# Kernel tuning notes

Measured on AMD Instinct MI355X. Metric: run time of the kernel, lower is better.

Reference implementation:

```python
import jax, jax.numpy as jnp
import numpy as np

N = 100000   # nodes
E = 1600000  # edges
D = 64       # hidden_channels
H = 2 * D    # MLP expansion
L = 4        # num_layers
G = 64       # graphs in batch
OUT = 1      # out_channels
LN_EPS = 1e-5


def layer_norm(h, gamma, beta):
    mu = jnp.mean(h, axis=-1, keepdims=True)
    var = jnp.var(h, axis=-1, keepdims=True)
    return (h - mu) * jax.lax.rsqrt(var + LN_EPS) * gamma + beta


def setup_inputs() -> dict:
    key = jax.random.key(0)
    ks = jax.random.split(key, 16)
    s = 0.05
    x = jax.random.normal(ks[0], (N, D), jnp.float32)
    edge_index = jax.random.randint(ks[1], (2, E), 0, N)
    batch = jnp.sort(jax.random.randint(ks[2], (N,), 0, G))
    # lin_in
    W_in = jax.random.normal(ks[3], (D, D), jnp.float32) * s
    b_in = jnp.zeros((D,), jnp.float32)
    # per-layer GINConv params (stacked over L layers)
    eps = jnp.zeros((L,), jnp.float32)
    W1 = jax.random.normal(ks[4], (L, D, H), jnp.float32) * s
    b1 = jnp.zeros((L, H), jnp.float32)
    gamma = jnp.ones((L, H), jnp.float32)
    beta = jnp.zeros((L, H), jnp.float32)
    W2 = jax.random.normal(ks[5], (L, H, D), jnp.float32) * s
    b2 = jnp.zeros((L, D), jnp.float32)
    # lin_out MLP
    Wo1 = jax.random.normal(ks[6], (D, H), jnp.float32) * s
    bo1 = jnp.zeros((H,), jnp.float32)
    Wo2 = jax.random.normal(ks[7], (H, OUT), jnp.float32) * s
    bo2 = jnp.zeros((OUT,), jnp.float32)
    return {
        "x": x, "W_in": W_in, "b_in": b_in, "eps": eps,
        "W1": W1, "b1": b1, "gamma": gamma, "beta": beta,
        "W2": W2, "b2": b2, "Wo1": Wo1, "bo1": bo1,
        "Wo2": Wo2, "bo2": bo2,
        "edge_index": edge_index, "batch": batch,
    }


def gin_conv(h, edge_index, eps_l, W1_l, b1_l, gamma_l, beta_l, W2_l, b2_l):
    src = edge_index[0]  # x_j
    dst = edge_index[1]  # aggregation target i
    # message = relu(x_j); aggr = scatter-add into dst
    agg = jax.ops.segment_sum(jax.nn.relu(h[src]), dst, num_segments=N)
    z = (1.0 + eps_l) * h + agg
    z = z @ W1_l + b1_l
    z = jax.nn.relu(layer_norm(z, gamma_l, beta_l))
    return z @ W2_l + b2_l


def reference(x, W_in, b_in, eps, W1, b1, gamma, beta, W2, b2,
              Wo1, bo1, Wo2, bo2, edge_index, batch):
    h = x @ W_in + b_in  # [N, D]
    for i in range(L):
        h = h + gin_conv(h, edge_index, eps[i], W1[i], b1[i],
                         gamma[i], beta[i], W2[i], b2[i])
        # dropout p=0.0 -> identity
    pooled = jax.ops.segment_sum(h, batch, num_segments=G)  # [G, D]
    out = jax.nn.relu(pooled @ Wo1 + bo1) @ Wo2 + bo2        # [G, OUT]
    return out.reshape(-1)
```

## Files before the change

### kernel.cpp

```cpp
#include <hip/hip_runtime.h>
#include <hip/hip_bf16.h>

#define NN 100000
#define NE 1600000
#define DD 64
#define HH 128
#define NLAYERS 4
#define NGRAPH 64
#define NBUCKET 782
#define NCHUNK 391
#define NTOT (NBUCKET * NCHUNK)

typedef __attribute__((ext_vector_type(8))) short bf16x8;
typedef __attribute__((ext_vector_type(4))) float f32x4;
typedef __attribute__((ext_vector_type(2))) float f32x2;

__device__ inline unsigned short bf16bits(float v) {
  return __bfloat16_as_ushort(__float2bfloat16(v));
}
__device__ inline float lo16(unsigned int u) { return __uint_as_float(u << 16); }
__device__ inline float hi16(unsigned int u) { return __uint_as_float(u & 0xFFFF0000u); }
__device__ inline float b2f(unsigned short u) { return __uint_as_float(((unsigned int)u) << 16); }


__global__ void k_hist(const int* __restrict__ dst, int* __restrict__ hist) {
  __shared__ int lh[NBUCKET];
  int t = threadIdx.x;
  int blk = blockIdx.x;
  for (int i = t; i < NBUCKET; i += 256) lh[i] = 0;
  __syncthreads();
  int cb = blk * 4096;
  int end = min(cb + 4096, NE);
  for (int i = cb + t; i < end; i += 256)
    atomicAdd(&lh[dst[i] >> 7], 1);
  __syncthreads();
  for (int i = t; i < NBUCKET; i += 256)
    hist[i * NCHUNK + blk] = lh[i];
}

__global__ void k_scan1(const int* __restrict__ in, int* __restrict__ out,
                        int* __restrict__ bsum, int n) {
  __shared__ int s[256];
  int t = threadIdx.x;
  int i = blockIdx.x * 256 + t;
  int v = (i < n) ? in[i] : 0;
  s[t] = v;
  __syncthreads();
  for (int off = 1; off < 256; off <<= 1) {
    int x = (t >= off) ? s[t - off] : 0;
    __syncthreads();
    s[t] += x;
    __syncthreads();
  }
  if (i < n) out[i] = s[t] - v;
  if (t == 255) bsum[blockIdx.x] = s[255];
}

__global__ void k_scan2b(int* bsum, int nb) {
  __shared__ int s[256];
  int t = threadIdx.x;
  int base = t * 5;
  int v[5];
  int sum = 0;
#pragma unroll
  for (int j = 0; j < 5; j++) {
    int i = base + j;
    v[j] = (i < nb) ? bsum[i] : 0;
    sum += v[j];
  }
  s[t] = sum;
  __syncthreads();
  for (int off = 1; off < 256; off <<= 1) {
    int x = (t >= off) ? s[t - off] : 0;
    __syncthreads();
    s[t] += x;
    __syncthreads();
  }
  int ex = s[t] - sum;
#pragma unroll
  for (int j = 0; j < 5; j++) {
    int i = base + j;
    if (i < nb) { int vv = v[j]; bsum[i] = ex; ex += vv; }
  }
}

__global__ void k_scan3b(int* __restrict__ hist, const int* __restrict__ bsum,
                         int* __restrict__ bbase, int n) {
  int i = blockIdx.x * 256 + threadIdx.x;
  if (i < n) {
    int v = hist[i] + bsum[i >> 8];
    hist[i] = v;
    if (i % NCHUNK == 0) bbase[i / NCHUNK] = v;
  }
}

__global__ void k_scatter(const int* __restrict__ src, const int* __restrict__ dst,
                          const int* __restrict__ hist, unsigned int* __restrict__ tmp) {
  __shared__ int lcur[NBUCKET];
  int t = threadIdx.x;
  int blk = blockIdx.x;
  for (int i = t; i < NBUCKET; i += 256) lcur[i] = hist[i * NCHUNK + blk];
  __syncthreads();
  int cb = blk * 4096;
  int end = min(cb + 4096, NE);
  for (int i = cb + t; i < end; i += 256) {
    int d = dst[i];
    int pos = atomicAdd(&lcur[d >> 7], 1);
    tmp[pos] = ((unsigned int)(d & 127) << 20) | (unsigned int)src[i];
  }
}

__global__ void k_fillB2(const unsigned int* __restrict__ tmp,
                         const int* __restrict__ bbase,
                         int* __restrict__ csr, int* __restrict__ offs,
                         int* __restrict__ cnt) {
  __shared__ int lcnt[128], lex[128], lcur[128];
  int b = blockIdx.x;
  int t = threadIdx.x;
  int base = bbase[b];
  int end = (b == NBUCKET - 1) ? NE : bbase[b + 1];
  if (t < 128) lcnt[t] = 0;
  __syncthreads();
  for (int i = base + t; i < end; i += 256)
    atomicAdd(&lcnt[tmp[i] >> 20], 1);
  __syncthreads();
  int v = (t < 128) ? lcnt[t] : 0;
  if (t < 128) lex[t] = v;
  __syncthreads();
  for (int off = 1; off < 128; off <<= 1) {
    int x = (t >= off && t < 128) ? lex[t - off] : 0;
    __syncthreads();
    if (t < 128) lex[t] += x;
    __syncthreads();
  }
  if (t < 128) {
    int ex = lex[t] - v;
    lcur[t] = ex;
    int node = (b << 7) + t;
    if (node < NN) { offs[node] = base + ex; cnt[node] = v; }
  }
  __syncthreads();
  for (int i = base + t; i < end; i += 256) {
    unsigned int u = tmp[i];
    int dl = u >> 20;
    int pos = atomicAdd(&lcur[dl], 1);
    csr[base + pos] = u & 0xFFFFF;
  }
}

__global__ void k_prep(const float* __restrict__ W1, const float* __restrict__ W2,
                       const float* __restrict__ W_in,
                       unsigned short* __restrict__ W1t, unsigned short* __restrict__ W2t,
                       unsigned short* __restrict__ Wint) {
  int bidx = blockIdx.x;
  int t = threadIdx.x;
  if (bidx == 2 * NLAYERS) {
    for (int i = t; i < 4096; i += 256) {
      int c = i >> 6, k = i & 63;
      Wint[i] = bf16bits(W_in[k * 64 + c]);
    }
    return;
  }
  int l = bidx >> 1;
  int m = bidx & 1;
  if (m == 0) {
    const float* src = W1 + (size_t)l * 8192;
    unsigned short* dstp = W1t + (size_t)l * 8192;
    for (int i = t; i < 8192; i += 256) {
      int c = i >> 6, k = i & 63;
      dstp[i] = bf16bits(src[k * 128 + c]);
    }
  } else {
    const float* src = W2 + (size_t)l * 8192;
    unsigned short* dstp = W2t + (size_t)l * 8192;
    for (int i = t; i < 8192; i += 256) {
      int c = i >> 7, k = i & 127;
      dstp[i] = bf16bits(src[k * 64 + c]);
    }
  }
}

__global__ __launch_bounds__(256) void k_lin(
    const float* __restrict__ x, const unsigned short* __restrict__ Wint,
    const float* __restrict__ binp, unsigned short* __restrict__ hout) {
  __shared__ __align__(16) unsigned short sW[4096];
  __shared__ float sb[64];
  int t = threadIdx.x;
  {
    const uint4* wg = (const uint4*)Wint;
    uint4* sWu = (uint4*)sW;
    for (int g = t; g < 512; g += 256) {
      int c = g >> 3, s = g & 7;
      sWu[c * 8 + (s ^ (c & 7))] = wg[g];
    }
    if (t < 64) sb[t] = binp[t];
  }
  int l = t & 63, w = t >> 6, lm = l & 15, lk = l >> 4;
  int rowl = w * 16 + lm;
  int grow = blockIdx.x * 64 + rowl;
  int growc = min(grow, NN - 1);
  bf16x8 a[2];
#pragma unroll
  for (int kb = 0; kb < 2; kb++) {
    const float* xp = &x[(size_t)growc * 64 + kb * 32 + lk * 8];
    float4 x0 = *(const float4*)xp;
    float4 x1 = *(const float4*)(xp + 4);
    a[kb][0] = (short)bf16bits(x0.x); a[kb][1] = (short)bf16bits(x0.y);
    a[kb][2] = (short)bf16bits(x0.z); a[kb][3] = (short)bf16bits(x0.w);
    a[kb][4] = (short)bf16bits(x1.x); a[kb][5] = (short)bf16bits(x1.y);
    a[kb][6] = (short)bf16bits(x1.z); a[kb][7] = (short)bf16bits(x1.w);
  }
  __syncthreads();
  f32x4 acc[4];
#pragma unroll
  for (int n = 0; n < 4; n++) {
    float bc = sb[n * 16 + lm];
    acc[n] = (f32x4){bc, bc, bc, bc};
  }
  const bf16x8* sWf = (const bf16x8*)sW;
#pragma unroll
  for (int n = 0; n < 4; n++) {
    int c = n * 16 + lm;
    bf16x8 b0 = sWf[c * 8 + ((0 * 4 + lk) ^ (c & 7))];
    bf16x8 b1 = sWf[c * 8 + ((1 * 4 + lk) ^ (c & 7))];
    acc[n] = __builtin_amdgcn_mfma_f32_16x16x32_bf16(a[0], b0, acc[n], 0, 0, 0);
    acc[n] = __builtin_amdgcn_mfma_f32_16x16x32_bf16(a[1], b1, acc[n], 0, 0, 0);
  }
#pragma unroll
  for (int r = 0; r < 4; r++) {
    int grow2 = blockIdx.x * 64 + w * 16 + lk * 4 + r;
    if (grow2 < NN) {
#pragma unroll
      for (int n = 0; n < 4; n++) {
        int c = n * 16 + lm;
        hout[(size_t)grow2 * 64 + c] = bf16bits(acc[n][r]);
      }
    }
  }
}

__global__ __launch_bounds__(256) void k_f8(const unsigned short* __restrict__ h,
                                            uint2* __restrict__ f8) {
  int i = blockIdx.x * 256 + threadIdx.x;
  if (i >= NN * 8) return;
  uint4 v = ((const uint4*)h)[i];
  float d0 = fmaxf(lo16(v.x), 0.f), d1 = fmaxf(hi16(v.x), 0.f);
  float d2 = fmaxf(lo16(v.y), 0.f), d3 = fmaxf(hi16(v.y), 0.f);
  float d4 = fmaxf(lo16(v.z), 0.f), d5 = fmaxf(hi16(v.z), 0.f);
  float d6 = fmaxf(lo16(v.w), 0.f), d7 = fmaxf(hi16(v.w), 0.f);
  int lo = 0, hi = 0;
  lo = __builtin_amdgcn_cvt_pk_fp8_f32(d0, d1, lo, false);
  lo = __builtin_amdgcn_cvt_pk_fp8_f32(d2, d3, lo, true);
  hi = __builtin_amdgcn_cvt_pk_fp8_f32(d4, d5, hi, false);
  hi = __builtin_amdgcn_cvt_pk_fp8_f32(d6, d7, hi, true);
  uint2 o;
  o.x = (unsigned int)lo;
  o.y = (unsigned int)hi;
  f8[i] = o;
}

__global__ __launch_bounds__(256) void k_fused(
    unsigned short* __restrict__ h, const uint2* __restrict__ f8v,
    const int* __restrict__ csr, const int* __restrict__ offs,
    const int* __restrict__ cnt,
    const unsigned short* __restrict__ W1t, const float* __restrict__ b1l,
    const float* __restrict__ gl, const float* __restrict__ btl,
    const unsigned short* __restrict__ W2t, const float* __restrict__ b2l,
    const float* __restrict__ epsl) {
  __shared__ __align__(16) unsigned short sW[8192];
  __shared__ __align__(16) unsigned short sRr[8192];
  __shared__ float sb1[128], sg[128], sbt[128], sb2[64];

  int t = threadIdx.x;
  int nbase = blockIdx.x * 64;
  int l = t & 63;
  int w = t >> 6;
  int lm = l & 15;
  int lk = l >> 4;

  {
    const uint4* w1g = (const uint4*)W1t;
    uint4* sWu = (uint4*)sW;
    for (int g = t; g < 1024; g += 256) {
      int c = g >> 3, s = g & 7;
      sWu[c * 8 + (s ^ (c & 7))] = w1g[g];
    }
    if (t < 128) { sb1[t] = b1l[t]; sg[t] = gl[t]; sbt[t] = btl[t]; }
    if (t < 64) sb2[t] = b2l[t];
  }
  float epsv = 1.0f + *epsl;

  int rowl = w * 16 + lm;
  int grow = nbase + rowl;
  int growc = min(grow, NN - 1);
  int start = offs[growc];
  int deg = (grow < NN) ? cnt[growc] : 0;

  const unsigned short* hp = h + (size_t)growc * 64 + lk * 8;
  uint4 hva = *(const uint4*)hp;
  uint4 hvb = *(const uint4*)(hp + 32);

  float accA[8] = {0.f, 0.f, 0.f, 0.f, 0.f, 0.f, 0.f, 0.f};
  float accB[8] = {0.f, 0.f, 0.f, 0.f, 0.f, 0.f, 0.f, 0.f};
  for (int j0 = 0; j0 < deg; j0 += 8) {
    int idxA = csr[start + j0 + lk];
    int idxB = csr[start + j0 + 4 + lk];
    int c8 = deg - j0;
    int ss[8];
#pragma unroll
    for (int jj = 0; jj < 4; jj++) ss[jj] = __shfl(idxA, lm + jj * 16);
#pragma unroll
    for (int jj = 0; jj < 4; jj++) ss[4 + jj] = __shfl(idxB, lm + jj * 16);
    uint2 va[8], vb[8];
#pragma unroll
    for (int jj = 0; jj < 8; jj++) {
      int s = (jj < c8) ? ss[jj] : ss[0];
      va[jj] = f8v[(size_t)s * 8 + lk];
      vb[jj] = f8v[(size_t)s * 8 + 4 + lk];
    }
#pragma unroll
    for (int jj = 0; jj < 8; jj++) {
      if (jj < c8) {
        f32x2 p;
        p = __builtin_amdgcn_cvt_pk_f32_fp8(va[jj].x, false); accA[0] += p.x; accA[1] += p.y;
        p = __builtin_amdgcn_cvt_pk_f32_fp8(va[jj].x, true);  accA[2] += p.x; accA[3] += p.y;
        p = __builtin_amdgcn_cvt_pk_f32_fp8(va[jj].y, false); accA[4] += p.x; accA[5] += p.y;
        p = __builtin_amdgcn_cvt_pk_f32_fp8(va[jj].y, true);  accA[6] += p.x; accA[7] += p.y;
        p = __builtin_amdgcn_cvt_pk_f32_fp8(vb[jj].x, false); accB[0] += p.x; accB[1] += p.y;
        p = __builtin_amdgcn_cvt_pk_f32_fp8(vb[jj].x, true);  accB[2] += p.x; accB[3] += p.y;
        p = __builtin_amdgcn_cvt_pk_f32_fp8(vb[jj].y, false); accB[4] += p.x; accB[5] += p.y;
        p = __builtin_amdgcn_cvt_pk_f32_fp8(vb[jj].y, true);  accB[6] += p.x; accB[7] += p.y;
      }
    }
  }

  bf16x8 a1[2];
  {
    float hz[8];
    hz[0] = lo16(hva.x); hz[1] = hi16(hva.x); hz[2] = lo16(hva.y); hz[3] = hi16(hva.y);
    hz[4] = lo16(hva.z); hz[5] = hi16(hva.z); hz[6] = lo16(hva.w); hz[7] = hi16(hva.w);
#pragma unroll
    for (int j = 0; j < 8; j++) a1[0][j] = (short)bf16bits(epsv * hz[j] + accA[j]);
    hz[0] = lo16(hvb.x); hz[1] = hi16(hvb.x); hz[2] = lo16(hvb.y); hz[3] = hi16(hvb.y);
    hz[4] = lo16(hvb.z); hz[5] = hi16(hvb.z); hz[6] = lo16(hvb.w); hz[7] = hi16(hvb.w);
#pragma unroll
    for (int j = 0; j < 8; j++) a1[1][j] = (short)bf16bits(epsv * hz[j] + accB[j]);
  }
  __syncthreads();

  f32x4 acc1[8];
#pragma unroll
  for (int n = 0; n < 8; n++) {
    float bc = sb1[n * 16 + lm];
    acc1[n] = (f32x4){bc, bc, bc, bc};
  }
  {
    const bf16x8* sW1f = (const bf16x8*)sW;
#pragma unroll
    for (int n = 0; n < 8; n++) {
      int c = n * 16 + lm;
      bf16x8 b0 = sW1f[c * 8 + ((0 * 4 + lk) ^ (c & 7))];
      bf16x8 b1f = sW1f[c * 8 + ((1 * 4 + lk) ^ (c & 7))];
      acc1[n] = __builtin_amdgcn_mfma_f32_16x16x32_bf16(a1[0], b0, acc1[n], 0, 0, 0);
      acc1[n] = __builtin_amdgcn_mfma_f32_16x16x32_bf16(a1[1], b1f, acc1[n], 0, 0, 0);
    }
  }

  float psr[4], pqr[4];
#pragma unroll
  for (int r = 0; r < 4; r++) {
    float s = 0.f, q = 0.f;
#pragma unroll
    for (int n = 0; n < 8; n++) { float v = acc1[n][r]; s += v; q += v * v; }
    psr[r] = s; pqr[r] = q;
  }
#pragma unroll
  for (int m = 1; m <= 8; m <<= 1) {
#pragma unroll
    for (int r = 0; r < 4; r++) {
      psr[r] += __shfl_xor(psr[r], m);
      pqr[r] += __shfl_xor(pqr[r], m);
    }
  }
#pragma unroll
  for (int r = 0; r < 4; r++) {
    float mu = psr[r] * (1.0f / 128.0f);
    float var = pqr[r] * (1.0f / 128.0f) - mu * mu;
    float rs = rsqrtf(var + 1e-5f);
    int rowr = w * 16 + lk * 4 + r;
#pragma unroll
    for (int n = 0; n < 8; n++) {
      int c = n * 16 + lm;
      float v = (acc1[n][r] - mu) * rs * sg[c] + sbt[c];
      v = fmaxf(v, 0.f);
      int slot = (c >> 3) ^ (rowr & 7);
      sRr[rowr * 128 + slot * 8 + (c & 7)] = bf16bits(v);
    }
  }
  __syncthreads();

  {
    const uint4* w2g = (const uint4*)W2t;
    uint4* sWu = (uint4*)sW;
    for (int g = t; g < 1024; g += 256) {
      int c = g >> 4, s = g & 15;
      sWu[c * 16 + (s ^ (c & 15))] = w2g[g];
    }
  }
  __syncthreads();

  f32x4 acc2[4];
#pragma unroll
  for (int n2 = 0; n2 < 4; n2++) {
    float bc = sb2[n2 * 16 + lm];
    acc2[n2] = (f32x4){bc, bc, bc, bc};
  }
  {
    const bf16x8* sRf = (const bf16x8*)sRr;
    const bf16x8* sW2f = (const bf16x8*)sW;
    bf16x8 a2[4];
#pragma unroll
    for (int kb = 0; kb < 4; kb++)
      a2[kb] = sRf[rowl * 16 + ((kb * 4 + lk) ^ (rowl & 7))];
#pragma unroll
    for (int n2 = 0; n2 < 4; n2++) {
      int c = n2 * 16 + lm;
#pragma unroll
      for (int kb = 0; kb < 4; kb++) {
        bf16x8 bfr = sW2f[c * 16 + ((kb * 4 + lk) ^ (c & 15))];
        acc2[n2] = __builtin_amdgcn_mfma_f32_16x16x32_bf16(a2[kb], bfr, acc2[n2], 0, 0, 0);
      }
    }
  }

#pragma unroll
  for (int r = 0; r < 4; r++) {
    int grow2 = nbase + w * 16 + lk * 4 + r;
    if (grow2 < NN) {
#pragma unroll
      for (int n2 = 0; n2 < 4; n2++) {
        int c = n2 * 16 + lm;
        size_t idx = (size_t)grow2 * 64 + c;
        float o = b2f(h[idx]) + acc2[n2][r];
        h[idx] = bf16bits(o);
      }
    }
  }
}

__global__ void k_pool(const unsigned short* __restrict__ h,
                       const int* __restrict__ batch,
                       float* __restrict__ pooled, int n) {
  int t = threadIdx.x;
  int d = t & 63;
  int w = t >> 6;
  int n0 = blockIdx.x * 256 + w * 64;
  float acc = 0.f;
  int prev = -1;
  for (int i = 0; i < 64; i++) {
    int nn = n0 + i;
    if (nn >= n) break;
    int g = batch[nn];
    if (g != prev) {
      if (prev >= 0) atomicAdd(&pooled[prev * 64 + d], acc);
      prev = g;
      acc = 0.f;
    }
    acc += b2f(h[(size_t)nn * 64 + d]);
  }
  if (prev >= 0) atomicAdd(&pooled[prev * 64 + d], acc);
}

__global__ __launch_bounds__(128) void k_out(
    const float* __restrict__ pooled, const float* __restrict__ Wo1,
    const float* __restrict__ bo1, const float* __restrict__ Wo2,
    const float* __restrict__ bo2, float* __restrict__ out) {
  __shared__ __align__(16) float sP[64];
  __shared__ float sPart[2];
  int g = blockIdx.x;
  int c = threadIdx.x;
  if (c < 64) sP[c] = pooled[g * 64 + c];
  __syncthreads();
  float t1 = bo1[c];
#pragma unroll 8
  for (int k = 0; k < 64; k++) t1 += sP[k] * Wo1[k * 128 + c];
  float v = fmaxf(t1, 0.f) * Wo2[c];
#pragma unroll
  for (int m = 1; m <= 32; m <<= 1) v += __shfl_xor(v, m);
  if ((c & 63) == 0) sPart[c >> 6] = v;
  __syncthreads();
  if (c == 0) out[g] = sPart[0] + sPart[1] + bo2[0];
}


static inline char* align_up(char* p, size_t a) {
  return (char*)(((uintptr_t)p + a - 1) & ~(uintptr_t)(a - 1));
}

extern "C" void kernel_launch(void* const* d_in, const int* in_sizes, int n_in,
                              void* d_out, int out_size, void* d_ws, size_t ws_size,
                              hipStream_t stream) {
  const float* x    = (const float*)d_in[0];
  const float* W_in = (const float*)d_in[1];
  const float* b_in = (const float*)d_in[2];
  const float* eps  = (const float*)d_in[3];
  const float* W1   = (const float*)d_in[4];
  const float* b1   = (const float*)d_in[5];
  const float* gam  = (const float*)d_in[6];
  const float* bet  = (const float*)d_in[7];
  const float* W2   = (const float*)d_in[8];
  const float* b2   = (const float*)d_in[9];
  const float* Wo1  = (const float*)d_in[10];
  const float* bo1  = (const float*)d_in[11];
  const float* Wo2  = (const float*)d_in[12];
  const float* bo2  = (const float*)d_in[13];
  const int* ei     = (const int*)d_in[14];
  const int* batch  = (const int*)d_in[15];
  float* out = (float*)d_out;

  const int* e_src = ei;
  const int* e_dst = ei + NE;

  char* p = (char*)d_ws;
  unsigned short* h = (unsigned short*)p;   p += (size_t)NN * 64 * 2;
  uint2* f8 = (uint2*)p;
  unsigned int* tmp = (unsigned int*)p;
                                            p += (size_t)NN * 64;
  int* csr = (int*)p;
  int* hist = (int*)p;
                                            p += (size_t)NE * 4;
  int* offs = (int*)p;                      p += (size_t)NN * 4;
  int* cnt = (int*)p;                       p += (size_t)NN * 4;
  int* bsumH = (int*)p;                     p += 1280 * 4;
  int* bbase = (int*)p;                     p += (NBUCKET + 1) * 4;
  p = align_up(p, 256);
  float* pooled = (float*)p;                p += (size_t)NGRAPH * 64 * 4;
  p = align_up(p, 256);
  unsigned short* W1t = (unsigned short*)p; p += (size_t)NLAYERS * 8192 * 2;
  unsigned short* W2t = (unsigned short*)p; p += (size_t)NLAYERS * 8192 * 2;
  unsigned short* Wint = (unsigned short*)p; p += 4096 * 2;

  const int SCAN_BLOCKS_H = (NTOT + 255) / 256;
  const int NODE_BLOCKS = (NN + 63) / 64;
  const int F8_BLOCKS = (NN * 8 + 255) / 256;

  hipMemsetAsync(pooled, 0, (size_t)NGRAPH * 64 * 4, stream);

  k_hist<<<NCHUNK, 256, 0, stream>>>(e_dst, hist);
  k_scan1<<<SCAN_BLOCKS_H, 256, 0, stream>>>(hist, hist, bsumH, NTOT);
  k_scan2b<<<1, 256, 0, stream>>>(bsumH, SCAN_BLOCKS_H);
  k_scan3b<<<SCAN_BLOCKS_H, 256, 0, stream>>>(hist, bsumH, bbase, NTOT);
  k_scatter<<<NCHUNK, 256, 0, stream>>>(e_src, e_dst, hist, tmp);
  k_fillB2<<<NBUCKET, 256, 0, stream>>>(tmp, bbase, csr, offs, cnt);

  k_prep<<<NLAYERS * 2 + 1, 256, 0, stream>>>(W1, W2, W_in, W1t, W2t, Wint);
  k_lin<<<NODE_BLOCKS, 256, 0, stream>>>(x, Wint, b_in, h);

  for (int l = 0; l < NLAYERS; l++) {
    k_f8<<<F8_BLOCKS, 256, 0, stream>>>(h, f8);
    k_fused<<<NODE_BLOCKS, 256, 0, stream>>>(h, f8, csr, offs, cnt,
        W1t + (size_t)l * 8192, b1 + (size_t)l * 128,
        gam + (size_t)l * 128, bet + (size_t)l * 128,
        W2t + (size_t)l * 8192, b2 + (size_t)l * 64,
        eps + l);
  }

  k_pool<<<(NN + 255) / 256, 256, 0, stream>>>(h, batch, pooled, NN);
  k_out<<<NGRAPH, 128, 0, stream>>>(pooled, Wo1, bo1, Wo2, bo2, out);
}
```

Measured before the change: 325.6 us.

## Fuse FP8 ReLU conversion into producer kernels with ping-pong buffers

New measurement: 314.5 us, median of 2. 1.04x faster.

```diff
diff --git a/kernel.cpp b/kernel.cpp
--- a/kernel.cpp
+++ b/kernel.cpp
@@ -8,7 +8,8 @@
 #define NLAYERS 4
 #define NGRAPH 64
 #define NBUCKET 782
-#define NCHUNK 391
+#define CHUNKSZ 8192
+#define NCHUNK 196
 #define NTOT (NBUCKET * NCHUNK)
 
 typedef __attribute__((ext_vector_type(8))) short bf16x8;
@@ -21,6 +22,10 @@
 __device__ inline float lo16(unsigned int u) { return __uint_as_float(u << 16); }
 __device__ inline float hi16(unsigned int u) { return __uint_as_float(u & 0xFFFF0000u); }
 __device__ inline float b2f(unsigned short u) { return __uint_as_float(((unsigned int)u) << 16); }
+__device__ inline unsigned char f8byte(float v) {
+  int pk = __builtin_amdgcn_cvt_pk_fp8_f32(fmaxf(v, 0.f), 0.f, 0, false);
+  return (unsigned char)(pk & 0xFF);
+}
 
 
 __global__ void k_hist(const int* __restrict__ dst, int* __restrict__ hist) {
@@ -29,8 +34,8 @@
   int blk = blockIdx.x;
   for (int i = t; i < NBUCKET; i += 256) lh[i] = 0;
   __syncthreads();
-  int cb = blk * 4096;
-  int end = min(cb + 4096, NE);
+  int cb = blk * CHUNKSZ;
+  int end = min(cb + CHUNKSZ, NE);
   for (int i = cb + t; i < end; i += 256)
     atomicAdd(&lh[dst[i] >> 7], 1);
   __syncthreads();
@@ -101,8 +106,8 @@
   int blk = blockIdx.x;
   for (int i = t; i < NBUCKET; i += 256) lcur[i] = hist[i * NCHUNK + blk];
   __syncthreads();
-  int cb = blk * 4096;
-  int end = min(cb + 4096, NE);
+  int cb = blk * CHUNKSZ;
+  int end = min(cb + CHUNKSZ, NE);
   for (int i = cb + t; i < end; i += 256) {
     int d = dst[i];
     int pos = atomicAdd(&lcur[d >> 7], 1);
@@ -182,7 +187,8 @@
 
 __global__ __launch_bounds__(256) void k_lin(
     const float* __restrict__ x, const unsigned short* __restrict__ Wint,
-    const float* __restrict__ binp, unsigned short* __restrict__ hout) {
+    const float* __restrict__ binp, unsigned short* __restrict__ hout,
+    unsigned char* __restrict__ f8out) {
   __shared__ __align__(16) unsigned short sW[4096];
   __shared__ float sb[64];
   int t = threadIdx.x;
@@ -233,34 +239,18 @@
 #pragma unroll
       for (int n = 0; n < 4; n++) {
         int c = n * 16 + lm;
-        hout[(size_t)grow2 * 64 + c] = bf16bits(acc[n][r]);
+        size_t idx = (size_t)grow2 * 64 + c;
+        float o = acc[n][r];
+        hout[idx] = bf16bits(o);
+        f8out[idx] = f8byte(o);
       }
     }
   }
 }
 
-__global__ __launch_bounds__(256) void k_f8(const unsigned short* __restrict__ h,
-                                            uint2* __restrict__ f8) {
-  int i = blockIdx.x * 256 + threadIdx.x;
-  if (i >= NN * 8) return;
-  uint4 v = ((const uint4*)h)[i];
-  float d0 = fmaxf(lo16(v.x), 0.f), d1 = fmaxf(hi16(v.x), 0.f);
-  float d2 = fmaxf(lo16(v.y), 0.f), d3 = fmaxf(hi16(v.y), 0.f);
-  float d4 = fmaxf(lo16(v.z), 0.f), d5 = fmaxf(hi16(v.z), 0.f);
-  float d6 = fmaxf(lo16(v.w), 0.f), d7 = fmaxf(hi16(v.w), 0.f);
-  int lo = 0, hi = 0;
-  lo = __builtin_amdgcn_cvt_pk_fp8_f32(d0, d1, lo, false);
-  lo = __builtin_amdgcn_cvt_pk_fp8_f32(d2, d3, lo, true);
-  hi = __builtin_amdgcn_cvt_pk_fp8_f32(d4, d5, hi, false);
-  hi = __builtin_amdgcn_cvt_pk_fp8_f32(d6, d7, hi, true);
-  uint2 o;
-  o.x = (unsigned int)lo;
-  o.y = (unsigned int)hi;
-  f8[i] = o;
-}
-
 __global__ __launch_bounds__(256) void k_fused(
-    unsigned short* __restrict__ h, const uint2* __restrict__ f8v,
+    unsigned short* __restrict__ h, const uint2* __restrict__ f8in,
+    unsigned char* __restrict__ f8out,
     const int* __restrict__ csr, const int* __restrict__ offs,
     const int* __restrict__ cnt,
     const unsigned short* __restrict__ W1t, const float* __restrict__ b1l,
@@ -315,8 +305,8 @@
 #pragma unroll
     for (int jj = 0; jj < 8; jj++) {
       int s = (jj < c8) ? ss[jj] : ss[0];
-      va[jj] = f8v[(size_t)s * 8 + lk];
-      vb[jj] = f8v[(size_t)s * 8 + 4 + lk];
+      va[jj] = f8in[(size_t)s * 8 + lk];
+      vb[jj] = f8in[(size_t)s * 8 + 4 + lk];
     }
 #pragma unroll
     for (int jj = 0; jj < 8; jj++) {
@@ -443,6 +433,7 @@
         size_t idx = (size_t)grow2 * 64 + c;
         float o = b2f(h[idx]) + acc2[n2][r];
         h[idx] = bf16bits(o);
+        f8out[idx] = f8byte(o);
       }
     }
   }
@@ -523,7 +514,8 @@
 
   char* p = (char*)d_ws;
   unsigned short* h = (unsigned short*)p;   p += (size_t)NN * 64 * 2;
-  uint2* f8 = (uint2*)p;
+  unsigned char* f8A = (unsigned char*)p;   p += (size_t)NN * 64;
+  unsigned char* f8B = (unsigned char*)p;
   unsigned int* tmp = (unsigned int*)p;
                                             p += (size_t)NN * 64;
   int* csr = (int*)p;
@@ -542,7 +534,6 @@
 
   const int SCAN_BLOCKS_H = (NTOT + 255) / 256;
   const int NODE_BLOCKS = (NN + 63) / 64;
-  const int F8_BLOCKS = (NN * 8 + 255) / 256;
 
   hipMemsetAsync(pooled, 0, (size_t)NGRAPH * 64 * 4, stream);
 
@@ -554,11 +545,12 @@
   k_fillB2<<<NBUCKET, 256, 0, stream>>>(tmp, bbase, csr, offs, cnt);
 
   k_prep<<<NLAYERS * 2 + 1, 256, 0, stream>>>(W1, W2, W_in, W1t, W2t, Wint);
-  k_lin<<<NODE_BLOCKS, 256, 0, stream>>>(x, Wint, b_in, h);
+  k_lin<<<NODE_BLOCKS, 256, 0, stream>>>(x, Wint, b_in, h, f8A);
 
   for (int l = 0; l < NLAYERS; l++) {
-    k_f8<<<F8_BLOCKS, 256, 0, stream>>>(h, f8);
-    k_fused<<<NODE_BLOCKS, 256, 0, stream>>>(h, f8, csr, offs, cnt,
+    const uint2* fin = (const uint2*)((l & 1) ? f8B : f8A);
+    unsigned char* fout = (l & 1) ? f8A : f8B;
+    k_fused<<<NODE_BLOCKS, 256, 0, stream>>>(h, fin, fout, csr, offs, cnt,
         W1t + (size_t)l * 8192, b1 + (size_t)l * 128,
         gam + (size_t)l * 128, bet + (size_t)l * 128,
         W2t + (size_t)l * 8192, b2 + (size_t)l * 64,
```
